# Optimization experiments

Measured on AMD Instinct MI355X. Metric: run time of the kernel, lower is better.

## Reference

```python
import jax, jax.numpy as jnp
import numpy as np

B, C_IN, N = 8, 3, 4096
H = [64, 128, 256]      # local conv widths
G = [128, 64]           # global MLP widths
K = 16                  # kNN neighbors for edge_conv
EPS = 1e-5


def _ln(x, g, b):
    # LayerNorm(num_point): normalize over the last (point) axis per channel
    mu = jnp.mean(x, axis=-1, keepdims=True)
    var = jnp.mean((x - mu) ** 2, axis=-1, keepdims=True)
    return (x - mu) / jnp.sqrt(var + EPS) * g + b


def _conv_ln_relu(x, w, b, g, be):
    # 1x1 Conv1d == per-point matmul: [B,Cin,N] -> [B,Cout,N]
    x = jnp.einsum('oi,bin->bon', w, x) + b[None, :, None]
    return jax.nn.relu(_ln(x, g, be))


def _edge_conv(x):
    # DGCNN-style edge conv: kNN in feature space, max-aggregate neighbor feats
    f = jnp.swapaxes(x, 1, 2)                                  # [B,N,C]
    sq = jnp.sum(f * f, axis=-1)                               # [B,N]
    d = sq[:, :, None] + sq[:, None, :] - 2.0 * jnp.einsum('bnc,bmc->bnm', f, f)
    _, idx = jax.lax.top_k(-jax.lax.stop_gradient(d), K)       # [B,N,K]
    nbr = jax.vmap(lambda fb, ib: fb[ib])(f, idx)              # [B,N,K,C] gather
    return jnp.swapaxes(jnp.max(nbr, axis=2), 1, 2)            # [B,C,N]


def setup_inputs() -> dict:
    key = jax.random.key(0)
    ks = jax.random.split(key, 20)
    inp = {"point_cloud": jax.random.normal(ks[0], (B, C_IN, N), jnp.float32)}
    prev = C_IN
    for i, h in enumerate(H):
        inp[f"w{i}"] = jax.random.normal(ks[1 + 3 * i], (h, prev), jnp.float32) * (1.0 / np.sqrt(prev))
        inp[f"b{i}"] = jnp.zeros((h,), jnp.float32)
        inp[f"g{i}"] = jnp.ones((N,), jnp.float32)
        inp[f"be{i}"] = jnp.zeros((N,), jnp.float32)
        prev = h
    for i, h in enumerate(G + [1]):
        inp[f"gw{i}"] = jax.random.normal(ks[10 + i], (h, prev), jnp.float32) * (1.0 / np.sqrt(prev))
        inp[f"gb{i}"] = jnp.zeros((h,), jnp.float32)
        prev = h
    return inp


def reference(point_cloud, w0, b0, g0, be0, w1, b1, g1, be1, w2, b2, g2, be2,
              gw0, gb0, gw1, gb1, gw2, gb2):
    x = _conv_ln_relu(point_cloud, w0, b0, g0, be0)
    x = _conv_ln_relu(x, w1, b1, g1, be1)
    x = _conv_ln_relu(x, w2, b2, g2, be2)
    x = _edge_conv(x)                      # [B,256,N]
    pooled = jnp.mean(x, axis=2)           # mean over points (pnt_axis=2)
    h = jax.nn.relu(pooled @ gw0.T + gb0)
    h = jax.nn.relu(h @ gw1.T + gb1)
    return h @ gw2.T + gb2                 # [B,1] energy
```

## Files before the change

### kernel.cpp

```cpp
#include <hip/hip_runtime.h>
#include <stdint.h>

#define NPTS 4096
#define BATCH 8
#define KNN 16

typedef __attribute__((ext_vector_type(8))) short short8;
typedef __attribute__((ext_vector_type(4))) float f32x4;
typedef unsigned long long u64;

template<int CIN, int G>
__global__ __launch_bounds__(256) void conv_ln_kernel(
    const float* __restrict__ X, const float* __restrict__ W,
    const float* __restrict__ bias, const float* __restrict__ g,
    const float* __restrict__ be, float* __restrict__ Y, int cout) {
    __shared__ float rows[G * NPTS];
    __shared__ double sh[256], sh2[256];
    int b = blockIdx.x;
    int co0 = blockIdx.y * G;
    int t = threadIdx.x;
    const float* xb = X + (size_t)b * CIN * NPTS;

#pragma unroll 1
    for (int chunk = 0; chunk < 4; ++chunk) {
        int n = chunk * 1024 + t * 4;
        f32x4 acc[G];
#pragma unroll
        for (int j = 0; j < G; ++j) {
            float bj = bias[co0 + j];
            acc[j] = (f32x4){bj, bj, bj, bj};
        }
        for (int ci = 0; ci < CIN; ++ci) {
            f32x4 xv = *(const f32x4*)(xb + (size_t)ci * NPTS + n);
#pragma unroll
            for (int j = 0; j < G; ++j) {
                float w = W[(co0 + j) * CIN + ci];
                acc[j].x = fmaf(w, xv.x, acc[j].x);
                acc[j].y = fmaf(w, xv.y, acc[j].y);
                acc[j].z = fmaf(w, xv.z, acc[j].z);
                acc[j].w = fmaf(w, xv.w, acc[j].w);
            }
        }
#pragma unroll
        for (int j = 0; j < G; ++j)
            *(f32x4*)(rows + j * NPTS + n) = acc[j];
    }
    __syncthreads();

#pragma unroll 1
    for (int j = 0; j < G; ++j) {
        float* row = rows + j * NPTS;
        double s = 0.0, s2 = 0.0;
        for (int i = t * 4; i < NPTS; i += 1024) {
            f32x4 v = *(const f32x4*)(row + i);
            s += (double)v.x + (double)v.y + (double)v.z + (double)v.w;
            s2 += (double)v.x * v.x + (double)v.y * v.y
                + (double)v.z * v.z + (double)v.w * v.w;
        }
        sh[t] = s; sh2[t] = s2;
        __syncthreads();
        for (int off = 128; off > 0; off >>= 1) {
            if (t < off) { sh[t] += sh[t + off]; sh2[t] += sh2[t + off]; }
            __syncthreads();
        }
        double mu = sh[0] / (double)NPTS;
        double var = sh2[0] / (double)NPTS - mu * mu;
        float rstd = (float)(1.0 / sqrt(var + 1e-5));
        float muf = (float)mu;
        float* yrow = Y + ((size_t)b * cout + co0 + j) * NPTS;
        for (int i = t * 4; i < NPTS; i += 1024) {
            f32x4 v = *(const f32x4*)(row + i);
            f32x4 gg = *(const f32x4*)(g + i);
            f32x4 bb = *(const f32x4*)(be + i);
            f32x4 o;
            o.x = fmaxf((v.x - muf) * rstd * gg.x + bb.x, 0.f);
            o.y = fmaxf((v.y - muf) * rstd * gg.y + bb.y, 0.f);
            o.z = fmaxf((v.z - muf) * rstd * gg.z + bb.z, 0.f);
            o.w = fmaxf((v.w - muf) * rstd * gg.w + bb.w, 0.f);
            *(f32x4*)(yrow + i) = o;
        }
        __syncthreads();
    }
}

#define ROW_E 72
#define ROW_B 144

__device__ inline unsigned short f2bf_rne(float x) {
    union { float f; unsigned u; } v; v.f = x;
    unsigned u = v.u;
    return (unsigned short)((u + 0x7FFFu + ((u >> 16) & 1u)) >> 16);
}

__global__ __launch_bounds__(256) void convert_kernel(
    const float* __restrict__ X2, unsigned short* __restrict__ Fc,
    float* __restrict__ SQ, float* __restrict__ Xt) {
    __shared__ float T[64][65];
    __shared__ float Q[64][4];
    int b = blockIdx.y;
    int n0 = blockIdx.x * 64;
    int t = threadIdx.x;
    int n_loc = t >> 2, cq = t & 3;
    int wave = t >> 6, lane = t & 63;
    float sacc = 0.f;
    for (int cc = 0; cc < 4; ++cc) {
        for (int r = 0; r < 16; ++r) {
            int cl = r * 4 + (t >> 6);
            T[cl][t & 63] = X2[((size_t)b * 256 + cc * 64 + cl) * NPTS + n0 + (t & 63)];
        }
        __syncthreads();
        if (Xt) {
#pragma unroll
            for (int r = 0; r < 16; ++r) {
                int n_l = wave * 16 + r;
                Xt[((size_t)b * NPTS + n0 + n_l) * 256 + cc * 64 + lane] = T[lane][n_l];
            }
        }
        size_t base = (((size_t)(b * 4 + cc) * NPTS) + n0 + n_loc) * ROW_E;
#pragma unroll
        for (int j = 0; j < 16; ++j) {
            int c = cq * 16 + j;
            float x = T[c][n_loc];
            sacc = fmaf(x, x, sacc);
            Fc[base + c] = f2bf_rne(x);
        }
        __syncthreads();
    }
    Q[n_loc][cq] = sacc;
    __syncthreads();
    if (t < 64)
        SQ[(size_t)b * NPTS + n0 + t] = Q[t][0] + Q[t][1] + Q[t][2] + Q[t][3];
}

#define A_BYTES 18432
#define BUF_B   36864
#define SENT32 0xFFFFFFFFu

__device__ inline void async_cp16(const void* g, void* l) {
    __builtin_amdgcn_global_load_lds((const __attribute__((address_space(1))) void*)g,
                                     (__attribute__((address_space(3))) void*)l, 16, 0, 0);
}

__device__ inline unsigned flip_f(float d) {
    union { float f; unsigned u; } v; v.f = d;
    return v.u ^ (((unsigned)((int)v.u >> 31)) | 0x80000000u);
}
__device__ inline float unflip_f(unsigned y) {
    unsigned m = (~((unsigned)((int)y >> 31))) | 0x80000000u;
    union { unsigned u; float f; } v; v.u = y ^ m;
    return v.f;
}
__device__ inline float thr_of(unsigned p) {
    unsigned tb = p | 0xFFFu;
    if (tb >= 0xFF800000u) tb = 0xFF800000u;
    return unflip_f(tb);
}

__global__ __launch_bounds__(256) void knn_mfma_kernel(
    const unsigned short* __restrict__ Fc, const float* __restrict__ SQ,
    unsigned* __restrict__ Dp) {
    __shared__ __align__(16) char smem[2 * BUF_B];
    __shared__ float sq_ks[128];
    __shared__ float thrx[256];
    int b = blockIdx.x;
    int q0 = blockIdx.y * 128;
    int ks = blockIdx.z;
    int t = threadIdx.x;
    int lane = t & 63;
    int wv = t >> 6;
    int wq = wv & 1, wk = wv >> 1;
    int quad = lane >> 4;
    int l15 = lane & 15;
    const float* sqb = SQ + (size_t)b * NPTS;
    const char* FcB = (const char*)Fc + (size_t)b * 4 * NPTS * ROW_B;

    thrx[t] = __int_as_float(0x7F800000);

    unsigned lst[KNN];
#pragma unroll
    for (int j = 0; j < KNN; ++j) lst[j] = SENT32;

    int q = t & 127, sub = t >> 7;

    {
        const char* gA = FcB + (size_t)q0 * ROW_B;
        const char* gB = FcB + (size_t)(ks * 2048) * ROW_B;
#pragma unroll
        for (int i = 0; i < 9; ++i) {
            int chunk = (i * 4 + wv) * 1024;
            const char* g = (chunk < A_BYTES) ? (gA + chunk) : (gB + (chunk - A_BYTES));
            async_cp16(g + lane * 16, smem + chunk);
        }
    }
    __syncthreads();

    for (int kt = 0; kt < 16; ++kt) {
        int kbase = ks * 2048 + kt * 128;
        if (t < 128) sq_ks[t] = sqb[kbase + t];
        f32x4 acc[4][4];
#pragma unroll
        for (int i = 0; i < 4; ++i)
#pragma unroll
            for (int j = 0; j < 4; ++j) acc[i][j] = (f32x4){0.f, 0.f, 0.f, 0.f};

#pragma unroll 1
        for (int kc = 0; kc < 4; ++kc) {
            int g = kt * 4 + kc;
            int gn = g + 1;
            if (gn < 64) {
                int kcn = gn & 3, ktn = gn >> 2;
                const char* gA = FcB + ((size_t)kcn * NPTS + q0) * ROW_B;
                const char* gB = FcB + ((size_t)kcn * NPTS + ks * 2048 + ktn * 128) * ROW_B;
                char* dst = smem + (gn & 1) * BUF_B;
#pragma unroll
                for (int i = 0; i < 9; ++i) {
                    int chunk = (i * 4 + wv) * 1024;
                    const char* gp = (chunk < A_BYTES) ? (gA + chunk) : (gB + (chunk - A_BYTES));
                    async_cp16(gp + lane * 16, dst + chunk);
                }
            }
            const char* base = smem + (g & 1) * BUF_B;
#pragma unroll
            for (int kss = 0; kss < 2; ++kss) {
                int coff = kss * 64 + quad * 16;
                short8 a[4], bf[4];
#pragma unroll
                for (int tq = 0; tq < 4; ++tq)
                    a[tq] = *(const short8*)(base + (wq * 64 + tq * 16 + l15) * ROW_B + coff);
#pragma unroll
                for (int tk = 0; tk < 4; ++tk)
                    bf[tk] = *(const short8*)(base + A_BYTES + (wk * 64 + tk * 16 + l15) * ROW_B + coff);
#pragma unroll
                for (int tq = 0; tq < 4; ++tq)
#pragma unroll
                    for (int tk = 0; tk < 4; ++tk)
                        acc[tq][tk] = __builtin_amdgcn_mfma_f32_16x16x32_bf16(
                            a[tq], bf[tk], acc[tq][tk], 0, 0, 0);
            }
            __syncthreads();
        }

        float* Gd = (float*)(smem + BUF_B);
        const float* gq = Gd + (size_t)q * 68 + sub * 32;
#pragma unroll 1
        for (int h = 0; h < 2; ++h) {
            if (wk == h) {
#pragma unroll
                for (int tk = 0; tk < 4; ++tk) {
                    float sqk = sq_ks[h * 64 + tk * 16 + l15];
#pragma unroll
                    for (int tq = 0; tq < 4; ++tq) {
                        float* gp = Gd + (size_t)(wq * 64 + tq * 16 + quad * 4) * 68
                                  + tk * 16 + l15;
                        f32x4 g = acc[tq][tk];
                        gp[0]   = fmaf(-2.f, g.x, sqk);
                        gp[68]  = fmaf(-2.f, g.y, sqk);
                        gp[136] = fmaf(-2.f, g.z, sqk);
                        gp[204] = fmaf(-2.f, g.w, sqk);
                    }
                }
            }
            __syncthreads();
            float thrf = fminf(thr_of(lst[KNN - 1]), thrx[t ^ 128]);
            unsigned mask = 0;
#pragma unroll
            for (int i = 7; i >= 0; --i) {
                f32x4 v = *(const f32x4*)(gq + i * 4);
                mask = mask + mask + (unsigned)(v.w <= thrf);
                mask = mask + mask + (unsigned)(v.z <= thrf);
                mask = mask + mask + (unsigned)(v.y <= thrf);
                mask = mask + mask + (unsigned)(v.x <= thrf);
            }
            while (__any((int)(mask != 0u))) {
                if (mask) {
                    int j = __ffs(mask) - 1;
                    mask &= mask - 1u;
                    float d = gq[j];
                    unsigned pk = (flip_f(d) & 0xFFFFF000u)
                                | (unsigned)(kbase + h * 64 + sub * 32 + j);
                    if (pk < lst[KNN - 1]) {
                        lst[KNN - 1] = pk;
#pragma unroll
                        for (int s = KNN - 1; s > 0; --s) {
                            if (lst[s] < lst[s - 1]) {
                                unsigned tmp = lst[s]; lst[s] = lst[s - 1]; lst[s - 1] = tmp;
                            }
                        }
                    }
                }
            }
            thrx[t] = thr_of(lst[KNN - 1]);
            __syncthreads();
        }
    }

    unsigned* mls = (unsigned*)smem;
#pragma unroll
    for (int j = 0; j < KNN; ++j) mls[t * 17 + j] = lst[j];
    __syncthreads();
    if (t < 128) {
        const unsigned* da = mls + t * 17;
        const unsigned* db = mls + (t + 128) * 17;
        unsigned* outp = Dp + ((size_t)((b * NPTS + q0 + t) * 2 + ks)) * KNN;
        int ia = 0, ib2 = 0;
        for (int k = 0; k < KNN; ++k) {
            bool ta = (ib2 >= KNN) || (ia < KNN && da[ia] < db[ib2]);
            outp[k] = ta ? da[ia++] : db[ib2++];
        }
    }
}

__global__ __launch_bounds__(256) void transpose_kernel(
    const float* __restrict__ X2, float* __restrict__ Xt) {
    __shared__ float T[64][65];
    int b = blockIdx.x;
    int n0 = blockIdx.y * 64;
    int t = threadIdx.x;
    int wave = t >> 6, lane = t & 63;
    for (int cc = 0; cc < 4; ++cc) {
        for (int r = 0; r < 16; ++r) {
            int cl = r * 4 + (t >> 6);
            T[cl][t & 63] = X2[((size_t)b * 256 + cc * 64 + cl) * NPTS + n0 + (t & 63)];
        }
        __syncthreads();
#pragma unroll
        for (int r = 0; r < 16; ++r) {
            int n_l = wave * 16 + r;
            Xt[((size_t)b * NPTS + n0 + n_l) * 256 + cc * 64 + lane] = T[lane][n_l];
        }
        __syncthreads();
    }
}

__global__ __launch_bounds__(256) void gather_pool_kernel(
    const float* __restrict__ Xt, const unsigned* __restrict__ Dp,
    float* __restrict__ Pp) {
    __shared__ int idxs[16][KNN];
    int b = blockIdx.x, blk = blockIdx.y;
    int t = threadIdx.x;
    if (t < 16) {
        int qg = b * NPTS + blk * 16 + t;
        const unsigned* L0 = Dp + (size_t)qg * 2 * KNN;
        const unsigned* L1 = L0 + KNN;
        int p0 = 0, p1 = 0;
#pragma unroll 1
        for (int k = 0; k < KNN; ++k) {
            bool ta = (p1 >= KNN) || (p0 < KNN && L0[p0] < L1[p1]);
            idxs[t][k] = (int)((ta ? L0[p0++] : L1[p1++]) & 0xFFFu);
        }
    }
    __syncthreads();
    int wv = t >> 6, lane = t & 63;
    const float* xb = Xt + (size_t)b * NPTS * 256;
    f32x4 sum = (f32x4){0.f, 0.f, 0.f, 0.f};
#pragma unroll 1
    for (int i = 0; i < 4; ++i) {
        const int* idp = idxs[wv * 4 + i];
        f32x4 m = *(const f32x4*)(xb + (size_t)idp[0] * 256 + lane * 4);
#pragma unroll
        for (int k = 1; k < KNN; ++k) {
            f32x4 v = *(const f32x4*)(xb + (size_t)idp[k] * 256 + lane * 4);
            m.x = fmaxf(m.x, v.x); m.y = fmaxf(m.y, v.y);
            m.z = fmaxf(m.z, v.z); m.w = fmaxf(m.w, v.w);
        }
        sum.x += m.x; sum.y += m.y; sum.z += m.z; sum.w += m.w;
    }
    __shared__ float S[4][256];
    *(f32x4*)&S[wv][lane * 4] = sum;
    __syncthreads();
    Pp[((size_t)b * 256 + blk) * 256 + t] = S[0][t] + S[1][t] + S[2][t] + S[3][t];
}

__global__ __launch_bounds__(256) void pool_mlp_kernel(
    const float* __restrict__ Pp,
    const float* __restrict__ gw0, const float* __restrict__ gb0,
    const float* __restrict__ gw1, const float* __restrict__ gb1,
    const float* __restrict__ gw2, const float* __restrict__ gb2,
    float* __restrict__ out) {
    __shared__ float P[256];
    __shared__ float h1[128];
    __shared__ float h2[64];
    int b = blockIdx.x, t = threadIdx.x;
    double s = 0.0;
#pragma unroll 4
    for (int j = 0; j < 256; ++j) s += (double)Pp[((size_t)b * 256 + j) * 256 + t];
    P[t] = (float)(s / (double)NPTS);
    __syncthreads();
    if (t < 128) {
        const float* w = gw0 + t * 256;
        double acc = 0.0;
        for (int c = 0; c < 256; ++c) acc += (double)P[c] * (double)w[c];
        float v = gb0[t] + (float)acc;
        h1[t] = v > 0.f ? v : 0.f;
    }
    __syncthreads();
    if (t < 64) {
        const float* w = gw1 + t * 128;
        double acc = 0.0;
        for (int c = 0; c < 128; ++c) acc += (double)h1[c] * (double)w[c];
        float v = gb1[t] + (float)acc;
        h2[t] = v > 0.f ? v : 0.f;
    }
    __syncthreads();
    if (t == 0) {
        double acc = 0.0;
        for (int c = 0; c < 64; ++c) acc += (double)h2[c] * (double)gw2[c];
        out[b] = gb2[0] + (float)acc;
    }
}

extern "C" void kernel_launch(void* const* d_in, const int* in_sizes, int n_in,
                              void* d_out, int out_size, void* d_ws, size_t ws_size,
                              hipStream_t stream) {
    const float* pc  = (const float*)d_in[0];
    const float* w0  = (const float*)d_in[1];
    const float* b0  = (const float*)d_in[2];
    const float* g0  = (const float*)d_in[3];
    const float* be0 = (const float*)d_in[4];
    const float* w1  = (const float*)d_in[5];
    const float* b1  = (const float*)d_in[6];
    const float* g1  = (const float*)d_in[7];
    const float* be1 = (const float*)d_in[8];
    const float* w2  = (const float*)d_in[9];
    const float* b2  = (const float*)d_in[10];
    const float* g2  = (const float*)d_in[11];
    const float* be2 = (const float*)d_in[12];
    const float* gw0 = (const float*)d_in[13];
    const float* gb0 = (const float*)d_in[14];
    const float* gw1 = (const float*)d_in[15];
    const float* gb1 = (const float*)d_in[16];
    const float* gw2 = (const float*)d_in[17];
    const float* gb2 = (const float*)d_in[18];
    float* out = (float*)d_out;

    float* ws = (float*)d_ws;
    float* X0 = ws;
    float* X2 = X0 + 2097152;
    float* R  = X2 + 8388608;
    float* X1 = R;
    unsigned short* Fc = (unsigned short*)R;
    unsigned* Dp = (unsigned*)X0;
    float* SQ = R + 11534336;
    float* P  = SQ + 32768;
    float* Pp = P + 2048;
    float* Xt2 = Pp + 524288;

    bool roomy = ws_size >= (size_t)(22579200ull + 8388608ull) * 4ull;
    float* Xt = roomy ? Xt2 : R;

    conv_ln_kernel<3, 2><<<dim3(BATCH, 64 / 2), 256, 0, stream>>>(
        pc, w0, b0, g0, be0, X0, 64);
    conv_ln_kernel<64, 4><<<dim3(BATCH, 128 / 4), 256, 0, stream>>>(
        X0, w1, b1, g1, be1, X1, 128);
    conv_ln_kernel<128, 4><<<dim3(BATCH, 256 / 4), 256, 0, stream>>>(
        X1, w2, b2, g2, be2, X2, 256);

    convert_kernel<<<dim3(NPTS / 64, BATCH), 256, 0, stream>>>(
        X2, Fc, SQ, roomy ? Xt2 : nullptr);
    knn_mfma_kernel<<<dim3(BATCH, 32, 2), 256, 0, stream>>>(Fc, SQ, Dp);
    if (!roomy)
        transpose_kernel<<<dim3(BATCH, NPTS / 64), 256, 0, stream>>>(X2, Xt);
    gather_pool_kernel<<<dim3(BATCH, 256), 256, 0, stream>>>(Xt, Dp, Pp);
    pool_mlp_kernel<<<dim3(BATCH), 256, 0, stream>>>(Pp, gw0, gb0, gw1, gb1, gw2, gb2, out);
}
```

Measured before the change: 440.5 us.

## Merge kNN candidate insertion into a single top-k list per query

```diff
diff --git a/kernel.cpp b/kernel.cpp
--- a/kernel.cpp
+++ b/kernel.cpp
@@ -161,7 +161,8 @@
     unsigned* __restrict__ Dp) {
     __shared__ __align__(16) char smem[2 * BUF_B];
     __shared__ float sq_ks[128];
-    __shared__ float thrx[256];
+    __shared__ float thrx[128];
+    __shared__ unsigned msk[256];
     int b = blockIdx.x;
     int q0 = blockIdx.y * 128;
     int ks = blockIdx.z;
@@ -174,7 +175,7 @@
     const float* sqb = SQ + (size_t)b * NPTS;
     const char* FcB = (const char*)Fc + (size_t)b * 4 * NPTS * ROW_B;
 
-    thrx[t] = __int_as_float(0x7F800000);
+    if (t < 128) thrx[t] = __int_as_float(0x7F800000);
 
     unsigned lst[KNN];
 #pragma unroll
@@ -261,7 +262,7 @@
                 }
             }
             __syncthreads();
-            float thrf = fminf(thr_of(lst[KNN - 1]), thrx[t ^ 128]);
+            float thrf = (t < 128) ? thr_of(lst[KNN - 1]) : thrx[q];
             unsigned mask = 0;
 #pragma unroll
             for (int i = 7; i >= 0; --i) {
@@ -271,42 +272,41 @@
                 mask = mask + mask + (unsigned)(v.y <= thrf);
                 mask = mask + mask + (unsigned)(v.x <= thrf);
             }
-            while (__any((int)(mask != 0u))) {
-                if (mask) {
-                    int j = __ffs(mask) - 1;
-                    mask &= mask - 1u;
-                    float d = gq[j];
-                    unsigned pk = (flip_f(d) & 0xFFFFF000u)
-                                | (unsigned)(kbase + h * 64 + sub * 32 + j);
-                    if (pk < lst[KNN - 1]) {
-                        lst[KNN - 1] = pk;
-#pragma unroll
-                        for (int s = KNN - 1; s > 0; --s) {
-                            if (lst[s] < lst[s - 1]) {
-                                unsigned tmp = lst[s]; lst[s] = lst[s - 1]; lst[s - 1] = tmp;
+            msk[t] = mask;
+            __syncthreads();
+            if (t < 128) {
+                unsigned m0 = mask;
+                unsigned m1 = msk[t + 128];
+                const float* gq0 = Gd + (size_t)t * 68;
+                while (__any((int)((m0 | m1) != 0u))) {
+                    if (m0 | m1) {
+                        int col;
+                        if (m0) { int j = __ffs(m0) - 1; m0 &= m0 - 1u; col = j; }
+                        else    { int j = __ffs(m1) - 1; m1 &= m1 - 1u; col = 32 + j; }
+                        float d = gq0[col];
+                        unsigned pk = (flip_f(d) & 0xFFFFF000u)
+                                    | (unsigned)(kbase + h * 64 + col);
+                        if (pk < lst[KNN - 1]) {
+                            lst[KNN - 1] = pk;
+#pragma unroll
+                            for (int s = KNN - 1; s > 0; --s) {
+                                if (lst[s] < lst[s - 1]) {
+                                    unsigned tmp = lst[s]; lst[s] = lst[s - 1]; lst[s - 1] = tmp;
+                                }
                             }
                         }
                     }
                 }
-            }
-            thrx[t] = thr_of(lst[KNN - 1]);
+                thrx[t] = thr_of(lst[KNN - 1]);
+            }
             __syncthreads();
         }
     }
 
-    unsigned* mls = (unsigned*)smem;
-#pragma unroll
-    for (int j = 0; j < KNN; ++j) mls[t * 17 + j] = lst[j];
-    __syncthreads();
     if (t < 128) {
-        const unsigned* da = mls + t * 17;
-        const unsigned* db = mls + (t + 128) * 17;
         unsigned* outp = Dp + ((size_t)((b * NPTS + q0 + t) * 2 + ks)) * KNN;
-        int ia = 0, ib2 = 0;
-        for (int k = 0; k < KNN; ++k) {
-            bool ta = (ib2 >= KNN) || (ia < KNN && da[ia] < db[ib2]);
-            outp[k] = ta ? da[ia++] : db[ib2++];
-        }
+#pragma unroll
+        for (int k = 0; k < KNN; ++k) outp[k] = lst[k];
     }
 }
 
```

Measured after the change: 462.3 us. 4.9% more time.
